# Kernel tuning notes

Measured on AMD Instinct MI355X. Metric: run time of the kernel, lower is better.

## Reference

```python
import jax, jax.numpy as jnp
import numpy as np


def setup_inputs() -> dict:
    key = jax.random.key(0)
    k1, k2, k3, k4, k5 = jax.random.split(key, 5)
    B, L, D = 8, 4096, 64
    return {
        "Q": jax.random.normal(k1, (B, L, D), dtype=jnp.float32),
        "K": jax.random.normal(k2, (B, L, D), dtype=jnp.float32),
        "V": jax.random.normal(k3, (B, L, D), dtype=jnp.float32),
        "sent_embed_slice": jax.random.normal(k4, (B, D), dtype=jnp.float32),
        "proj": jax.random.normal(k5, (D, D), dtype=jnp.float32),  # fixed phi projection (M, d)
        "qkv_size": 64,
        "masked": 1,
    }


def _phi(X, proj, M):
    # X: (B, L, d). Original applies phi per timestep slice x = X[:, t, :] of shape (B, d)
    # phi(x) = (1/sqrt(M)) * exp(-0.5 * ||x||_F) * exp(proj @ x), Frobenius norm over the (B, d) slice.
    logits = jnp.einsum("bld,md->blm", X, proj)            # (B, L, M)
    scale = jnp.exp(-0.5 * jnp.sqrt(jnp.sum(X * X, axis=(0, 2))))  # per-timestep scalar, (L,)
    return jnp.exp(logits) * scale[None, :, None] / jnp.sqrt(jnp.asarray(M, jnp.float32))


def reference(Q, K, V, sent_embed_slice, proj, qkv_size, masked):
    M = qkv_size
    phi_q = _phi(Q, proj, M)  # (B, L, M)
    phi_k = _phi(K, proj, M)  # (B, L, M)
    if masked:
        # causal running sums: KV_t = sum_{j<=t} phi_k_j outer V_j ; N_t = sum_{j<=t} phi_k_j
        KV = jnp.cumsum(phi_k[:, :, :, None] * V[:, :, None, :], axis=1)  # (B, L, M, D)
        Nc = jnp.cumsum(phi_k, axis=1)                                    # (B, L, M)
        num = jnp.einsum("blm,blmd->bld", phi_q, KV)
        r = jnp.einsum("blm,blm->bl", phi_q, Nc)
        return num / (r + jnp.sign(r) * 1e-6)[:, :, None]
    else:
        KV = jnp.einsum("blm,bld->bmd", phi_k, V)     # (B, M, D)
        Ns = jnp.sum(phi_k, axis=1)                    # (B, M); broadcast over D like torch norm_sum
        num = jnp.einsum("blm,bmd->bld", phi_q, KV)
        r = jnp.einsum("blm,bm->bl", phi_q, Ns)
        return num / r[:, :, None]
```

## Files before the change

### kernel.cpp

```cpp
#include <hip/hip_runtime.h>
#include <math.h>

#define BB 8
#define LL 4096
#define DD 64
#define SS 64
#define NCHUNK 64
#define STATE 4160

typedef __attribute__((ext_vector_type(8))) short s16x8;
typedef __attribute__((ext_vector_type(8))) unsigned short u16x8;
typedef __attribute__((ext_vector_type(4))) float f32x4;

#define MFMA(a, b, c) __builtin_amdgcn_mfma_f32_16x16x32_bf16((a), (b), (c), 0, 0, 0)

static __device__ __forceinline__ unsigned short f2bf(float x) {
  unsigned int u = __builtin_bit_cast(unsigned int, x);
  u += 0x7FFFu + ((u >> 16) & 1u);
  return (unsigned short)(u >> 16);
}
static __device__ __forceinline__ float bf2f(unsigned short h) {
  unsigned int u = ((unsigned int)h) << 16;
  return __builtin_bit_cast(float, u);
}

static __device__ __forceinline__ s16x8 ld_frag(const unsigned short* base, int row0, int ks) {
  const int lane = threadIdx.x & 63;
  const int r = row0 + (lane & 15);
  const int idx = r * 64 + ((ks * 32 + ((lane & 48) >> 1)) ^ ((r & 7) << 3));
  return *(const s16x8*)(base + idx);
}

static __device__ __forceinline__ void stage_hl(unsigned short* __restrict__ Sh,
                                                unsigned short* __restrict__ Sl,
                                                const float* __restrict__ src, int tid) {
#pragma unroll
  for (int it = 0; it < 2; ++it) {
    const int g = tid + it * 256;
    const int row = g >> 3;
    const int c0 = (g & 7) * 8;
    const float4 x0 = *(const float4*)(src + row * 64 + c0);
    const float4 x1 = *(const float4*)(src + row * 64 + c0 + 4);
    const float xs[8] = {x0.x, x0.y, x0.z, x0.w, x1.x, x1.y, x1.z, x1.w};
    u16x8 h, l;
#pragma unroll
    for (int k = 0; k < 8; ++k) {
      const unsigned short hh = f2bf(xs[k]);
      h[k] = hh;
      l[k] = f2bf(xs[k] - bf2f(hh));
    }
    const int idx = row * 64 + (c0 ^ ((row & 7) << 3));
    *(u16x8*)(Sh + idx) = h;
    *(u16x8*)(Sl + idx) = l;
  }
}

static __device__ __forceinline__ void logits3(const unsigned short* Ah_, const unsigned short* Al_,
                                               const unsigned short* Bh_, const unsigned short* Bl_,
                                               int w, f32x4 acc[4]) {
  s16x8 ah[2], al[2];
#pragma unroll
  for (int ks = 0; ks < 2; ++ks) {
    ah[ks] = ld_frag(Ah_, w * 16, ks);
    al[ks] = ld_frag(Al_, w * 16, ks);
  }
#pragma unroll
  for (int ct = 0; ct < 4; ++ct) {
#pragma unroll
    for (int ks = 0; ks < 2; ++ks) {
      const s16x8 bh = ld_frag(Bh_, ct * 16, ks);
      const s16x8 bl = ld_frag(Bl_, ct * 16, ks);
      acc[ct] = MFMA(ah[ks], bh, acc[ct]);
      acc[ct] = MFMA(ah[ks], bl, acc[ct]);
      acc[ct] = MFMA(al[ks], bh, acc[ct]);
    }
  }
}

static __device__ __forceinline__ void phi_store_row(unsigned short* dst, const f32x4* acc,
                                                     const float* sc, int w) {
  const int lane = threadIdx.x & 63;
#pragma unroll
  for (int ri = 0; ri < 4; ++ri) {
    const int t = w * 16 + ((lane & 48) >> 2) + ri;
#pragma unroll
    for (int ct = 0; ct < 4; ++ct) {
      const int m = ct * 16 + (lane & 15);
      dst[t * 64 + (m ^ ((t & 7) << 3))] = f2bf(__expf(acc[ct][ri]) * sc[ri]);
    }
  }
}

static __device__ __forceinline__ void phi_store_col(unsigned short* dst, const f32x4* acc,
                                                     const float* sc, int w) {
  const int lane = threadIdx.x & 63;
#pragma unroll
  for (int ri = 0; ri < 4; ++ri) {
    const int t = w * 16 + ((lane & 48) >> 2) + ri;
#pragma unroll
    for (int ct = 0; ct < 4; ++ct) {
      const int m = ct * 16 + (lane & 15);
      dst[m * 64 + (t ^ ((m & 7) << 3))] = f2bf(__expf(acc[ct][ri]) * sc[ri]);
    }
  }
}

static __device__ __forceinline__ void stage_vhalf(float* __restrict__ F, const float* __restrict__ src,
                                                   int tid) {
#pragma unroll
  for (int it = 0; it < 2; ++it) {
    const int g = tid + it * 256;
    const int row = g >> 4;
    const int col = (g & 15) * 4;
    *(float4*)(F + row * 64 + col) = *(const float4*)(src + row * 64 + col);
  }
}

static __device__ __forceinline__ void stage_vfull(float* __restrict__ F, const float* __restrict__ src,
                                                   int tid) {
#pragma unroll
  for (int it = 0; it < 4; ++it) {
    const int g = tid + it * 256;
    const int row = g >> 4;
    const int col = (g & 15) * 4;
    *(float4*)(F + row * 64 + col) = *(const float4*)(src + row * 64 + col);
  }
}

static __device__ __forceinline__ void vtrans_half(unsigned short* __restrict__ Gh,
                                                   unsigned short* __restrict__ Hl,
                                                   const float* __restrict__ F, int tid, int half) {
  const int d = tid & 63;
  const int tb = (tid >> 6) * 8;
  float v[8];
#pragma unroll
  for (int k = 0; k < 8; ++k) v[k] = F[(tb + k) * 64 + d];
  u16x8 hh, ll;
#pragma unroll
  for (int k = 0; k < 8; ++k) {
    const unsigned short h = f2bf(v[k]);
    hh[k] = h;
    ll[k] = f2bf(v[k] - bf2f(h));
  }
  const int idx = d * 64 + ((half * 32 + tb) ^ ((d & 7) << 3));
  *(u16x8*)(Gh + idx) = hh;
  *(u16x8*)(Hl + idx) = ll;
}

__global__ __launch_bounds__(256) void k_scales(const float* __restrict__ Q,
                                                const float* __restrict__ K,
                                                float* __restrict__ ws) {
  const int t = blockIdx.x * 4 + (threadIdx.x >> 6);
  const int lane = threadIdx.x & 63;
  const int b = lane >> 3;
  const int d0 = (lane & 7) * 8;
  const size_t base = (size_t)b * (LL * DD) + (size_t)t * DD + d0;
  float sq = 0.f, sk = 0.f;
#pragma unroll
  for (int k = 0; k < 8; ++k) {
    const float q = Q[base + k]; sq += q * q;
    const float kk = K[base + k]; sk += kk * kk;
  }
#pragma unroll
  for (int off = 32; off; off >>= 1) {
    sq += __shfl_xor(sq, off);
    sk += __shfl_xor(sk, off);
  }
  if (lane == 0) {
    ws[t]      = expf(-0.5f * sqrtf(sq));
    ws[LL + t] = expf(-0.5f * sqrtf(sk));
  }
}

__global__ __launch_bounds__(256) void k_phi_sums(const float* __restrict__ Qg,
                                                  const float* __restrict__ Kg,
                                                  const float* __restrict__ Vg,
                                                  const float* __restrict__ proj,
                                                  const float* __restrict__ ws,
                                                  float* __restrict__ states,
                                                  unsigned short* __restrict__ phiQg,
                                                  unsigned short* __restrict__ phiKg) {
  __shared__ unsigned short P0[4096], P1[4096];
  __shared__ unsigned short X0[4096], X1[4096];
  __shared__ unsigned short Y0[4096], Y1[4096];
  __shared__ unsigned short PHIr[4096];
  __shared__ unsigned short PHIc[4096];
  __shared__ float F[2048];
  const int tid = threadIdx.x;
  const int lane = tid & 63;
  const int w = tid >> 6;
  const int bc = blockIdx.x;
  const int b = bc >> 6;
  const int c = bc & (NCHUNK - 1);
  const int t0 = c * SS;
  const size_t tileBase = ((size_t)b * LL + t0) * DD;
  float* stc = states + ((size_t)b * NCHUNK + c) * (size_t)STATE;
  unsigned short* pqT = phiQg + (size_t)bc * 4096;
  unsigned short* pkT = phiKg + (size_t)bc * 4096;

  stage_hl(P0, P1, proj, tid);
  stage_hl(X0, X1, Qg + tileBase, tid);
  stage_hl(Y0, Y1, Kg + tileBase, tid);
  stage_vhalf(F, Vg + tileBase, tid);
  float scq[4], sck[4];
#pragma unroll
  for (int ri = 0; ri < 4; ++ri) {
    const int trow = w * 16 + ((lane & 48) >> 2) + ri;
    scq[ri] = ws[t0 + trow] * 0.125f;
    sck[ri] = ws[LL + t0 + trow] * 0.125f;
  }
  __syncthreads();

  {
    f32x4 acc[4] = {};
    logits3(X0, X1, P0, P1, w, acc);
    phi_store_row(X0, acc, scq, w);
  }
  {
    f32x4 acc[4] = {};
    logits3(Y0, Y1, P0, P1, w, acc);
    phi_store_row(PHIr, acc, sck, w);
    phi_store_col(PHIc, acc, sck, w);
  }
  __syncthreads();

  vtrans_half(Y0, Y1, F, tid, 0);
  {
    const int o = tid * 16;
    *(u16x8*)(pqT + o)     = *(const u16x8*)(X0 + o);
    *(u16x8*)(pqT + o + 8) = *(const u16x8*)(X0 + o + 8);
    *(u16x8*)(pkT + o)     = *(const u16x8*)(PHIr + o);
    *(u16x8*)(pkT + o + 8) = *(const u16x8*)(PHIr + o + 8);
  }
  {
    const int m = tid >> 2, q = tid & 3;
    float s = 0.f;
#pragma unroll
    for (int p = 0; p < 2; ++p) {
      const int tt = q * 16 + p * 8;
      const u16x8 vv = *(const u16x8*)(PHIc + m * 64 + (tt ^ ((m & 7) << 3)));
#pragma unroll
      for (int i = 0; i < 8; ++i) s += bf2f(vv[i]);
    }
    s += __shfl_xor(s, 1);
    s += __shfl_xor(s, 2);
    if (q == 0) stc[4096 + m] = s;
  }
  __syncthreads();
  stage_vhalf(F, Vg + tileBase + 32 * 64, tid);
  __syncthreads();
  vtrans_half(Y0, Y1, F, tid, 1);
  __syncthreads();

  {
    s16x8 avh[2], avl[2];
#pragma unroll
    for (int ks = 0; ks < 2; ++ks) {
      avh[ks] = ld_frag(Y0, w * 16, ks);
      avl[ks] = ld_frag(Y1, w * 16, ks);
    }
    f32x4 acc[4] = {};
#pragma unroll
    for (int ct = 0; ct < 4; ++ct) {
#pragma unroll
      for (int ks = 0; ks < 2; ++ks) {
        const s16x8 bp = ld_frag(PHIc, ct * 16, ks);
        acc[ct] = MFMA(avh[ks], bp, acc[ct]);
        acc[ct] = MFMA(avl[ks], bp, acc[ct]);
      }
    }
#pragma unroll
    for (int ri = 0; ri < 4; ++ri) {
      const int d = w * 16 + ((lane & 48) >> 2) + ri;
#pragma unroll
      for (int ct = 0; ct < 4; ++ct) {
        stc[d * 64 + ct * 16 + (lane & 15)] = acc[ct][ri];
      }
    }
  }
}

__global__ __launch_bounds__(256) void k_prefix1(const float* __restrict__ states,
                                                 float* __restrict__ tmp) {
  const int e = blockIdx.x * 256 + threadIdx.x;
  if (e >= BB * 8 * STATE) return;
  const int b = e / (8 * STATE);
  const int r = e % (8 * STATE);
  const int g = r / STATE;
  const int el = r % STATE;
  const float* p = states + ((size_t)b * NCHUNK + g * 8) * STATE + el;
  float s = 0.f;
#pragma unroll
  for (int i = 0; i < 8; ++i) s += p[(size_t)i * STATE];
  tmp[((size_t)b * 8 + g) * STATE + el] = s;
}

__global__ __launch_bounds__(256) void k_prefix2(float* __restrict__ states,
                                                 const float* __restrict__ tmp) {
  const int e = blockIdx.x * 256 + threadIdx.x;
  if (e >= BB * 8 * STATE) return;
  const int b = e / (8 * STATE);
  const int r = e % (8 * STATE);
  const int g = r / STATE;
  const int el = r % STATE;
  float run = 0.f;
  for (int g2 = 0; g2 < g; ++g2) run += tmp[((size_t)b * 8 + g2) * STATE + el];
  float* p = states + ((size_t)b * NCHUNK + g * 8) * STATE + el;
#pragma unroll
  for (int i = 0; i < 8; ++i) {
    const float v = p[(size_t)i * STATE];
    p[(size_t)i * STATE] = run;
    run += v;
  }
}

__global__ __launch_bounds__(256) void k_out(const float* __restrict__ Vg,
                                             const unsigned short* __restrict__ phiQg,
                                             const unsigned short* __restrict__ phiKg,
                                             const float* __restrict__ states,
                                             float* __restrict__ out) {
  __shared__ unsigned short PQ[4096];
  __shared__ unsigned short PK[4096];
  __shared__ unsigned short E[4096];
  __shared__ unsigned short KV0[4096], KV1[4096];
  __shared__ unsigned short VT0[4096], VT1[4096];
  __shared__ float F[4096];
  const int tid = threadIdx.x;
  const int lane = tid & 63;
  const int w = tid >> 6;
  const int bc = blockIdx.x;
  const int b = bc >> 6;
  const int c = bc & (NCHUNK - 1);
  const int t0 = c * SS;
  const size_t tileBase = ((size_t)b * LL + t0) * DD;
  const float* st = states + ((size_t)b * NCHUNK + c) * (size_t)STATE;
  const unsigned short* pqT = phiQg + (size_t)bc * 4096;
  const unsigned short* pkT = phiKg + (size_t)bc * 4096;

  {
    const int o = tid * 16;
    *(u16x8*)(PQ + o)     = *(const u16x8*)(pqT + o);
    *(u16x8*)(PQ + o + 8) = *(const u16x8*)(pqT + o + 8);
    *(u16x8*)(PK + o)     = *(const u16x8*)(pkT + o);
    *(u16x8*)(PK + o + 8) = *(const u16x8*)(pkT + o + 8);
  }
  stage_hl(KV0, KV1, st, tid);
  stage_vfull(F, Vg + tileBase, tid);
  __syncthreads();

  vtrans_half(VT0, VT1, F, tid, 0);
  vtrans_half(VT0, VT1, F + 32 * 64, tid, 1);

  float rsI[4];
  s16x8 aq[2];
#pragma unroll
  for (int ks = 0; ks < 2; ++ks) aq[ks] = ld_frag(PQ, w * 16, ks);
  {
    f32x4 accA[4] = {};
#pragma unroll
    for (int ct = 0; ct < 4; ++ct) {
#pragma unroll
      for (int ks = 0; ks < 2; ++ks) {
        accA[ct] = MFMA(aq[ks], ld_frag(PK, ct * 16, ks), accA[ct]);
      }
    }
#pragma unroll
    for (int ri = 0; ri < 4; ++ri) {
      const int t = w * 16 + ((lane & 48) >> 2) + ri;
      float part = 0.f;
#pragma unroll
      for (int ct = 0; ct < 4; ++ct) {
        const int j = ct * 16 + (lane & 15);
        const float a = (j <= t) ? accA[ct][ri] : 0.f;
        const unsigned short ah = f2bf(a);
        part += bf2f(ah);
        E[t * 64 + (j ^ ((t & 7) << 3))] = ah;
      }
#pragma unroll
      for (int off = 1; off < 16; off <<= 1) part += __shfl_xor(part, off);
      rsI[ri] = part;
    }
  }
  __syncthreads();

  {
    s16x8 aA[2];
#pragma unroll
    for (int ks = 0; ks < 2; ++ks) aA[ks] = ld_frag(E, w * 16, ks);
    f32x4 acc[4] = {};
#pragma unroll
    for (int ct = 0; ct < 4; ++ct) {
#pragma unroll
      for (int ks = 0; ks < 2; ++ks) {
        acc[ct] = MFMA(aA[ks], ld_frag(VT0, ct * 16, ks), acc[ct]);
        acc[ct] = MFMA(aA[ks], ld_frag(VT1, ct * 16, ks), acc[ct]);
        acc[ct] = MFMA(aq[ks], ld_frag(KV0, ct * 16, ks), acc[ct]);
        acc[ct] = MFMA(aq[ks], ld_frag(KV1, ct * 16, ks), acc[ct]);
      }
    }
    float rsp = 0.f;
    const float* Np = st + 4096;
#pragma unroll
    for (int ks = 0; ks < 2; ++ks) {
      const int m0 = ks * 32 + ((lane & 48) >> 1);
      const float4 n0 = *(const float4*)(Np + m0);
      const float4 n1 = *(const float4*)(Np + m0 + 4);
      const float nn[8] = {n0.x, n0.y, n0.z, n0.w, n1.x, n1.y, n1.z, n1.w};
#pragma unroll
      for (int i = 0; i < 8; ++i) rsp += bf2f((unsigned short)aq[ks][i]) * nn[i];
    }
    rsp += __shfl_xor(rsp, 16);
    rsp += __shfl_xor(rsp, 32);
#pragma unroll
    for (int ri = 0; ri < 4; ++ri) {
      const float r = rsI[ri] + __shfl(rsp, ((lane & 48) >> 2) + ri);
      const float inv = 1.f / (r + copysignf(1e-6f, r));
      const int t = w * 16 + ((lane & 48) >> 2) + ri;
#pragma unroll
      for (int ct = 0; ct < 4; ++ct) {
        out[tileBase + t * 64 + ct * 16 + (lane & 15)] = acc[ct][ri] * inv;
      }
    }
  }
}

extern "C" void kernel_launch(void* const* d_in, const int* in_sizes, int n_in,
                              void* d_out, int out_size, void* d_ws, size_t ws_size,
                              hipStream_t stream) {
  (void)in_sizes; (void)n_in; (void)out_size; (void)ws_size;
  const float* Q    = (const float*)d_in[0];
  const float* K    = (const float*)d_in[1];
  const float* V    = (const float*)d_in[2];
  const float* proj = (const float*)d_in[4];
  float* out = (float*)d_out;
  float* ws  = (float*)d_ws;
  float* states = ws + 2 * LL;
  const size_t statesFloats = (size_t)BB * NCHUNK * STATE;
  float* tmp = states + statesFloats;
  const size_t tmpFloats = (size_t)BB * 8 * STATE;
  unsigned short* phiQg = (unsigned short*)(tmp + tmpFloats);
  unsigned short* phiKg = phiQg + (size_t)BB * NCHUNK * 4096;

  hipLaunchKernelGGL(k_scales, dim3(LL / 4), dim3(256), 0, stream, Q, K, ws);
  hipLaunchKernelGGL(k_phi_sums, dim3(BB * NCHUNK), dim3(256), 0, stream,
                     Q, K, V, proj, ws, states, phiQg, phiKg);
  hipLaunchKernelGGL(k_prefix1, dim3((BB * 8 * STATE + 255) / 256), dim3(256), 0, stream, states, tmp);
  hipLaunchKernelGGL(k_prefix2, dim3((BB * 8 * STATE + 255) / 256), dim3(256), 0, stream, states, tmp);
  hipLaunchKernelGGL(k_out, dim3(BB * NCHUNK), dim3(256), 0, stream,
                     V, phiQg, phiKg, states, out);
}
```

Baseline: 35.78 us.

## Load MFMA fragments directly from global memory instead of staging through LDS

Both the phi/chunk-sum kernel and the output kernel now build MFMA operand fragments straight from global memory in registers, doing the hi/lo bf16 split in registers rather than staging Q, K, V, proj, the states and phi tiles through shared memory. This removes most LDS buffers, several __syncthreads and the LDS transpose of V, which cuts shared-memory footprint and should raise occupancy. The trade-off is redundant and strided global loads: the V transpose reads scalar columns, and proj and V fragments are re-read by every wave, so the kernels lean on cache hits.

```diff
diff --git a/kernel.cpp b/kernel.cpp
--- a/kernel.cpp
+++ b/kernel.cpp
@@ -24,6 +24,7 @@
   return __builtin_bit_cast(float, u);
 }
 
+
 static __device__ __forceinline__ s16x8 ld_frag(const unsigned short* base, int row0, int ks) {
   const int lane = threadIdx.x & 63;
   const int r = row0 + (lane & 15);
@@ -31,49 +32,40 @@
   return *(const s16x8*)(base + idx);
 }
 
-static __device__ __forceinline__ void stage_hl(unsigned short* __restrict__ Sh,
-                                                unsigned short* __restrict__ Sl,
-                                                const float* __restrict__ src, int tid) {
-#pragma unroll
-  for (int it = 0; it < 2; ++it) {
-    const int g = tid + it * 256;
-    const int row = g >> 3;
-    const int c0 = (g & 7) * 8;
-    const float4 x0 = *(const float4*)(src + row * 64 + c0);
-    const float4 x1 = *(const float4*)(src + row * 64 + c0 + 4);
-    const float xs[8] = {x0.x, x0.y, x0.z, x0.w, x1.x, x1.y, x1.z, x1.w};
-    u16x8 h, l;
-#pragma unroll
-    for (int k = 0; k < 8; ++k) {
-      const unsigned short hh = f2bf(xs[k]);
-      h[k] = hh;
-      l[k] = f2bf(xs[k] - bf2f(hh));
-    }
-    const int idx = row * 64 + (c0 ^ ((row & 7) << 3));
-    *(u16x8*)(Sh + idx) = h;
-    *(u16x8*)(Sl + idx) = l;
-  }
-}
-
-static __device__ __forceinline__ void logits3(const unsigned short* Ah_, const unsigned short* Al_,
-                                               const unsigned short* Bh_, const unsigned short* Bl_,
-                                               int w, f32x4 acc[4]) {
-  s16x8 ah[2], al[2];
-#pragma unroll
-  for (int ks = 0; ks < 2; ++ks) {
-    ah[ks] = ld_frag(Ah_, w * 16, ks);
-    al[ks] = ld_frag(Al_, w * 16, ks);
-  }
-#pragma unroll
-  for (int ct = 0; ct < 4; ++ct) {
-#pragma unroll
-    for (int ks = 0; ks < 2; ++ks) {
-      const s16x8 bh = ld_frag(Bh_, ct * 16, ks);
-      const s16x8 bl = ld_frag(Bl_, ct * 16, ks);
-      acc[ct] = MFMA(ah[ks], bh, acc[ct]);
-      acc[ct] = MFMA(ah[ks], bl, acc[ct]);
-      acc[ct] = MFMA(al[ks], bh, acc[ct]);
-    }
+static __device__ __forceinline__ void ldg_hl(const float* __restrict__ G, int row0, int ks,
+                                              s16x8& h, s16x8& l) {
+  const int lane = threadIdx.x & 63;
+  const int r = row0 + (lane & 15);
+  const int k0 = ks * 32 + ((lane & 48) >> 1);
+  const float4 a = *(const float4*)(G + r * 64 + k0);
+  const float4 b = *(const float4*)(G + r * 64 + k0 + 4);
+  const float xs[8] = {a.x, a.y, a.z, a.w, b.x, b.y, b.z, b.w};
+#pragma unroll
+  for (int i = 0; i < 8; ++i) {
+    const unsigned short hh = f2bf(xs[i]);
+    h[i] = (short)hh;
+    l[i] = (short)f2bf(xs[i] - bf2f(hh));
+  }
+}
+
+static __device__ __forceinline__ s16x8 ldg_bf(const unsigned short* __restrict__ G, int row0, int ks) {
+  const int lane = threadIdx.x & 63;
+  const int r = row0 + (lane & 15);
+  const int k0 = ks * 32 + ((lane & 48) >> 1);
+  return *(const s16x8*)(G + r * 64 + k0);
+}
+
+static __device__ __forceinline__ void ldg_vt_hl(const float* __restrict__ V, int row0, int ks,
+                                                 s16x8& h, s16x8& l) {
+  const int lane = threadIdx.x & 63;
+  const int d = row0 + (lane & 15);
+  const int t0 = ks * 32 + ((lane & 48) >> 1);
+#pragma unroll
+  for (int i = 0; i < 8; ++i) {
+    const float v = V[(t0 + i) * 64 + d];
+    const unsigned short hh = f2bf(v);
+    h[i] = (short)hh;
+    l[i] = (short)f2bf(v - bf2f(hh));
   }
 }
 
@@ -103,48 +95,6 @@
       dst[m * 64 + (t ^ ((m & 7) << 3))] = f2bf(__expf(acc[ct][ri]) * sc[ri]);
     }
   }
-}
-
-static __device__ __forceinline__ void stage_vhalf(float* __restrict__ F, const float* __restrict__ src,
-                                                   int tid) {
-#pragma unroll
-  for (int it = 0; it < 2; ++it) {
-    const int g = tid + it * 256;
-    const int row = g >> 4;
-    const int col = (g & 15) * 4;
-    *(float4*)(F + row * 64 + col) = *(const float4*)(src + row * 64 + col);
-  }
-}
-
-static __device__ __forceinline__ void stage_vfull(float* __restrict__ F, const float* __restrict__ src,
-                                                   int tid) {
-#pragma unroll
-  for (int it = 0; it < 4; ++it) {
-    const int g = tid + it * 256;
-    const int row = g >> 4;
-    const int col = (g & 15) * 4;
-    *(float4*)(F + row * 64 + col) = *(const float4*)(src + row * 64 + col);
-  }
-}
-
-static __device__ __forceinline__ void vtrans_half(unsigned short* __restrict__ Gh,
-                                                   unsigned short* __restrict__ Hl,
-                                                   const float* __restrict__ F, int tid, int half) {
-  const int d = tid & 63;
-  const int tb = (tid >> 6) * 8;
-  float v[8];
-#pragma unroll
-  for (int k = 0; k < 8; ++k) v[k] = F[(tb + k) * 64 + d];
-  u16x8 hh, ll;
-#pragma unroll
-  for (int k = 0; k < 8; ++k) {
-    const unsigned short h = f2bf(v[k]);
-    hh[k] = h;
-    ll[k] = f2bf(v[k] - bf2f(h));
-  }
-  const int idx = d * 64 + ((half * 32 + tb) ^ ((d & 7) << 3));
-  *(u16x8*)(Gh + idx) = hh;
-  *(u16x8*)(Hl + idx) = ll;
 }
 
 __global__ __launch_bounds__(256) void k_scales(const float* __restrict__ Q,
@@ -180,12 +130,9 @@
                                                   float* __restrict__ states,
                                                   unsigned short* __restrict__ phiQg,
                                                   unsigned short* __restrict__ phiKg) {
-  __shared__ unsigned short P0[4096], P1[4096];
-  __shared__ unsigned short X0[4096], X1[4096];
-  __shared__ unsigned short Y0[4096], Y1[4096];
-  __shared__ unsigned short PHIr[4096];
-  __shared__ unsigned short PHIc[4096];
-  __shared__ float F[2048];
+  __shared__ unsigned short PQ[4096];
+  __shared__ unsigned short PKr[4096];
+  __shared__ unsigned short PKc[4096];
   const int tid = threadIdx.x;
   const int lane = tid & 63;
   const int w = tid >> 6;
@@ -198,10 +145,16 @@
   unsigned short* pqT = phiQg + (size_t)bc * 4096;
   unsigned short* pkT = phiKg + (size_t)bc * 4096;
 
-  stage_hl(P0, P1, proj, tid);
-  stage_hl(X0, X1, Qg + tileBase, tid);
-  stage_hl(Y0, Y1, Kg + tileBase, tid);
-  stage_vhalf(F, Vg + tileBase, tid);
+  s16x8 vh[2], vl[2];
+#pragma unroll
+  for (int ks = 0; ks < 2; ++ks) ldg_vt_hl(Vg + tileBase, w * 16, ks, vh[ks], vl[ks]);
+
+  s16x8 ph[4][2], pl[4][2];
+#pragma unroll
+  for (int ct = 0; ct < 4; ++ct)
+#pragma unroll
+    for (int ks = 0; ks < 2; ++ks) ldg_hl(proj, ct * 16, ks, ph[ct][ks], pl[ct][ks]);
+
   float scq[4], sck[4];
 #pragma unroll
   for (int ri = 0; ri < 4; ++ri) {
@@ -209,28 +162,50 @@
     scq[ri] = ws[t0 + trow] * 0.125f;
     sck[ri] = ws[LL + t0 + trow] * 0.125f;
   }
+
+  {
+    s16x8 qh[2], ql[2];
+#pragma unroll
+    for (int ks = 0; ks < 2; ++ks) ldg_hl(Qg + tileBase, w * 16, ks, qh[ks], ql[ks]);
+    f32x4 acc[4] = {};
+#pragma unroll
+    for (int ct = 0; ct < 4; ++ct)
+#pragma unroll
+      for (int ks = 0; ks < 2; ++ks) {
+        acc[ct] = MFMA(qh[ks], ph[ct][ks], acc[ct]);
+        acc[ct] = MFMA(qh[ks], pl[ct][ks], acc[ct]);
+        acc[ct] = MFMA(ql[ks], ph[ct][ks], acc[ct]);
+      }
+    phi_store_row(PQ, acc, scq, w);
+  }
+  {
+    s16x8 kh[2], kl[2];
+#pragma unroll
+    for (int ks = 0; ks < 2; ++ks) ldg_hl(Kg + tileBase, w * 16, ks, kh[ks], kl[ks]);
+    f32x4 acc[4] = {};
+#pragma unroll
+    for (int ct = 0; ct < 4; ++ct)
+#pragma unroll
+      for (int ks = 0; ks < 2; ++ks) {
+        acc[ct] = MFMA(kh[ks], ph[ct][ks], acc[ct]);
+        acc[ct] = MFMA(kh[ks], pl[ct][ks], acc[ct]);
+        acc[ct] = MFMA(kl[ks], ph[ct][ks], acc[ct]);
+      }
+    phi_store_row(PKr, acc, sck, w);
+    phi_store_col(PKc, acc, sck, w);
+  }
   __syncthreads();
 
   {
-    f32x4 acc[4] = {};
-    logits3(X0, X1, P0, P1, w, acc);
-    phi_store_row(X0, acc, scq, w);
-  }
-  {
-    f32x4 acc[4] = {};
-    logits3(Y0, Y1, P0, P1, w, acc);
-    phi_store_row(PHIr, acc, sck, w);
-    phi_store_col(PHIc, acc, sck, w);
-  }
-  __syncthreads();
-
-  vtrans_half(Y0, Y1, F, tid, 0);
-  {
-    const int o = tid * 16;
-    *(u16x8*)(pqT + o)     = *(const u16x8*)(X0 + o);
-    *(u16x8*)(pqT + o + 8) = *(const u16x8*)(X0 + o + 8);
-    *(u16x8*)(pkT + o)     = *(const u16x8*)(PHIr + o);
-    *(u16x8*)(pkT + o + 8) = *(const u16x8*)(PHIr + o + 8);
+    const int r0 = tid >> 3;
+    const int c0 = (tid & 7) * 8;
+#pragma unroll
+    for (int it = 0; it < 2; ++it) {
+      const int r = r0 + it * 32;
+      const int sidx = r * 64 + (c0 ^ ((r & 7) << 3));
+      *(u16x8*)(pqT + r * 64 + c0) = *(const u16x8*)(PQ + sidx);
+      *(u16x8*)(pkT + r * 64 + c0) = *(const u16x8*)(PKr + sidx);
+    }
   }
   {
     const int m = tid >> 2, q = tid & 3;
@@ -238,7 +213,7 @@
 #pragma unroll
     for (int p = 0; p < 2; ++p) {
       const int tt = q * 16 + p * 8;
-      const u16x8 vv = *(const u16x8*)(PHIc + m * 64 + (tt ^ ((m & 7) << 3)));
+      const u16x8 vv = *(const u16x8*)(PKc + m * 64 + (tt ^ ((m & 7) << 3)));
 #pragma unroll
       for (int i = 0; i < 8; ++i) s += bf2f(vv[i]);
     }
@@ -246,29 +221,16 @@
     s += __shfl_xor(s, 2);
     if (q == 0) stc[4096 + m] = s;
   }
-  __syncthreads();
-  stage_vhalf(F, Vg + tileBase + 32 * 64, tid);
-  __syncthreads();
-  vtrans_half(Y0, Y1, F, tid, 1);
-  __syncthreads();
-
-  {
-    s16x8 avh[2], avl[2];
-#pragma unroll
-    for (int ks = 0; ks < 2; ++ks) {
-      avh[ks] = ld_frag(Y0, w * 16, ks);
-      avl[ks] = ld_frag(Y1, w * 16, ks);
-    }
+  {
     f32x4 acc[4] = {};
 #pragma unroll
-    for (int ct = 0; ct < 4; ++ct) {
-#pragma unroll
-      for (int ks = 0; ks < 2; ++ks) {
-        const s16x8 bp = ld_frag(PHIc, ct * 16, ks);
-        acc[ct] = MFMA(avh[ks], bp, acc[ct]);
-        acc[ct] = MFMA(avl[ks], bp, acc[ct]);
-      }
-    }
+    for (int ct = 0; ct < 4; ++ct)
+#pragma unroll
+      for (int ks = 0; ks < 2; ++ks) {
+        const s16x8 bp = ld_frag(PKc, ct * 16, ks);
+        acc[ct] = MFMA(vh[ks], bp, acc[ct]);
+        acc[ct] = MFMA(vl[ks], bp, acc[ct]);
+      }
 #pragma unroll
     for (int ri = 0; ri < 4; ++ri) {
       const int d = w * 16 + ((lane & 48) >> 2) + ri;
@@ -319,12 +281,7 @@
                                              const unsigned short* __restrict__ phiKg,
                                              const float* __restrict__ states,
                                              float* __restrict__ out) {
-  __shared__ unsigned short PQ[4096];
-  __shared__ unsigned short PK[4096];
   __shared__ unsigned short E[4096];
-  __shared__ unsigned short KV0[4096], KV1[4096];
-  __shared__ unsigned short VT0[4096], VT1[4096];
-  __shared__ float F[4096];
   const int tid = threadIdx.x;
   const int lane = tid & 63;
   const int w = tid >> 6;
@@ -337,33 +294,18 @@
   const unsigned short* pqT = phiQg + (size_t)bc * 4096;
   const unsigned short* pkT = phiKg + (size_t)bc * 4096;
 
-  {
-    const int o = tid * 16;
-    *(u16x8*)(PQ + o)     = *(const u16x8*)(pqT + o);
-    *(u16x8*)(PQ + o + 8) = *(const u16x8*)(pqT + o + 8);
-    *(u16x8*)(PK + o)     = *(const u16x8*)(pkT + o);
-    *(u16x8*)(PK + o + 8) = *(const u16x8*)(pkT + o + 8);
-  }
-  stage_hl(KV0, KV1, st, tid);
-  stage_vfull(F, Vg + tileBase, tid);
-  __syncthreads();
-
-  vtrans_half(VT0, VT1, F, tid, 0);
-  vtrans_half(VT0, VT1, F + 32 * 64, tid, 1);
+  s16x8 aq[2];
+#pragma unroll
+  for (int ks = 0; ks < 2; ++ks) aq[ks] = ldg_bf(pqT, w * 16, ks);
 
   float rsI[4];
-  s16x8 aq[2];
-#pragma unroll
-  for (int ks = 0; ks < 2; ++ks) aq[ks] = ld_frag(PQ, w * 16, ks);
   {
     f32x4 accA[4] = {};
 #pragma unroll
-    for (int ct = 0; ct < 4; ++ct) {
-#pragma unroll
-      for (int ks = 0; ks < 2; ++ks) {
-        accA[ct] = MFMA(aq[ks], ld_frag(PK, ct * 16, ks), accA[ct]);
-      }
-    }
+    for (int ct = 0; ct < 4; ++ct)
+#pragma unroll
+      for (int ks = 0; ks < 2; ++ks)
+        accA[ct] = MFMA(aq[ks], ldg_bf(pkT, ct * 16, ks), accA[ct]);
 #pragma unroll
     for (int ri = 0; ri < 4; ++ri) {
       const int t = w * 16 + ((lane & 48) >> 2) + ri;
@@ -390,12 +332,18 @@
     f32x4 acc[4] = {};
 #pragma unroll
     for (int ct = 0; ct < 4; ++ct) {
-#pragma unroll
-      for (int ks = 0; ks < 2; ++ks) {
-        acc[ct] = MFMA(aA[ks], ld_frag(VT0, ct * 16, ks), acc[ct]);
-        acc[ct] = MFMA(aA[ks], ld_frag(VT1, ct * 16, ks), acc[ct]);
-        acc[ct] = MFMA(aq[ks], ld_frag(KV0, ct * 16, ks), acc[ct]);
-        acc[ct] = MFMA(aq[ks], ld_frag(KV1, ct * 16, ks), acc[ct]);
+      s16x8 vth[2], vtl[2], kvh[2], kvl[2];
+#pragma unroll
+      for (int ks = 0; ks < 2; ++ks) {
+        ldg_vt_hl(Vg + tileBase, ct * 16, ks, vth[ks], vtl[ks]);
+        ldg_hl(st, ct * 16, ks, kvh[ks], kvl[ks]);
+      }
+#pragma unroll
+      for (int ks = 0; ks < 2; ++ks) {
+        acc[ct] = MFMA(aA[ks], vth[ks], acc[ct]);
+        acc[ct] = MFMA(aA[ks], vtl[ks], acc[ct]);
+        acc[ct] = MFMA(aq[ks], kvh[ks], acc[ct]);
+        acc[ct] = MFMA(aq[ks], kvl[ks], acc[ct]);
       }
     }
     float rsp = 0.f;
```

Result: slower. 41.14 us (+15.0%).
